# Optimization experiments

Hardware: AMD Instinct MI355X
Metric: run time of the kernel (lower is better)

## Reference

```python
import jax, jax.numpy as jnp
import numpy as np

NW, NS, E = 50000, 10000, 100000
H, C = 6, 300            # heads, out_channels (word_size)
DIN_S, DIN_W = 640, 300  # sentence_size, word_size
DHID = 2048              # FFN hidden


def setup_inputs() -> dict:
    key = jax.random.key(0)
    ks = jax.random.split(key, 12)
    Hw = jax.random.normal(ks[0], (NW, DIN_W), dtype=jnp.float32)
    Hs = jax.random.normal(ks[1], (NS, DIN_S), dtype=jnp.float32)
    src = jax.random.randint(ks[2], (E,), 0, NS)
    dst = jax.random.randint(ks[3], (E,), 0, NW)
    s2w = jnp.stack([src, dst]).astype(jnp.int64)  # [2, E] edge_index
    # GATConv params (bipartite): lin_src, lin_dst, att_src, att_dst, bias
    Wsrc = jax.random.normal(ks[4], (H * C, DIN_S), dtype=jnp.float32) / np.sqrt(DIN_S)
    Wdst = jax.random.normal(ks[5], (H * C, DIN_W), dtype=jnp.float32) / np.sqrt(DIN_W)
    att_src = jax.random.normal(ks[6], (H, C), dtype=jnp.float32) / np.sqrt(C)
    att_dst = jax.random.normal(ks[7], (H, C), dtype=jnp.float32) / np.sqrt(C)
    bias_gat = jnp.zeros((H * C,), dtype=jnp.float32)
    # FFN params: Linear(1800 -> 2048), Linear(2048 -> 300)
    W1 = jax.random.normal(ks[8], (DHID, H * C), dtype=jnp.float32) / np.sqrt(H * C)
    b1 = jnp.zeros((DHID,), dtype=jnp.float32)
    W2 = jax.random.normal(ks[9], (DIN_W, DHID), dtype=jnp.float32) / np.sqrt(DHID)
    b2 = jnp.zeros((DIN_W,), dtype=jnp.float32)
    return dict(Hw=Hw, Hs=Hs, s2w=s2w, Wsrc=Wsrc, Wdst=Wdst, att_src=att_src,
                att_dst=att_dst, bias_gat=bias_gat, W1=W1, b1=b1, W2=W2, b2=b2)


def reference(Hw, Hs, s2w, Wsrc, Wdst, att_src, att_dst, bias_gat, W1, b1, W2, b2):
    nw = Hw.shape[0]
    src, dst = s2w[0], s2w[1]
    h, c = att_src.shape
    # edge-wise linear transforms (done node-wise, then gathered)
    xs = (Hs @ Wsrc.T).reshape(-1, h, c)   # [Ns, H, C]
    xd = (Hw @ Wdst.T).reshape(-1, h, c)   # [Nw, H, C]
    a_s = jnp.einsum('nhc,hc->nh', xs, att_src)  # [Ns, H]
    a_d = jnp.einsum('nhc,hc->nh', xd, att_dst)  # [Nw, H]
    alpha = a_s[src] + a_d[dst]                  # [E, H]
    alpha = jnp.where(alpha > 0, alpha, 0.2 * alpha)  # leaky_relu(0.2)
    # segment softmax over edges grouped by destination word
    m = jax.ops.segment_max(alpha, dst, num_segments=nw)      # [Nw, H]
    ex = jnp.exp(alpha - m[dst])                               # [E, H]
    den = jax.ops.segment_sum(ex, dst, num_segments=nw)       # [Nw, H]
    w = ex / den[dst]                                          # [E, H]
    msg = xs[src] * w[:, :, None]                              # [E, H, C]
    agg = jax.ops.segment_sum(msg, dst, num_segments=nw)      # [Nw, H, C]
    Uw = agg.reshape(nw, h * c) + bias_gat                     # concat heads + bias
    # activation (elu), dropout treated as identity (deterministic reference)
    Uw = jax.nn.elu(Uw)
    # FFN with residual to Hw
    out = (Uw @ W1.T + b1) @ W2.T + b2 + Hw
    return out
```

## Files before the change

### kernel.cpp

```cpp
#include <hip/hip_runtime.h>
#include <hip/hip_bf16.h>
#include <math.h>

#define NWn 50000
#define NSn 10000
#define NEn 100000
#define Hn  6
#define DWn 300
#define DSn 640
#define DHn 2048
#define HCn 1800
#define HCp 1824
#define CHUNK 10000
#define ENC_NEGINF 0x007FFFFFu

typedef short bf16x8 __attribute__((ext_vector_type(8)));
typedef float f32x4  __attribute__((ext_vector_type(4)));

__device__ __forceinline__ unsigned enc_ord(float f) {
  unsigned u = __float_as_uint(f);
  return (u & 0x80000000u) ? ~u : (u | 0x80000000u);
}
__device__ __forceinline__ float dec_ord(unsigned u) {
  unsigned v = (u & 0x80000000u) ? (u ^ 0x80000000u) : ~u;
  return __uint_as_float(v);
}
__device__ __forceinline__ float eluf(float x) { return x > 0.0f ? x : expm1f(x); }
__device__ __forceinline__ float b2f(short s) {
  return __uint_as_float(((unsigned)(unsigned short)s) << 16);
}
__device__ __forceinline__ short f2b(float f) {
  __hip_bfloat16 h = __float2bfloat16(f);
  return *(short*)&h;
}

__device__ __forceinline__ int ld_src(const int* s32, int e, int f) {
  return f ? s32[2 * e] : s32[e];
}
__device__ __forceinline__ int ld_dst(const int* s32, int e, int f) {
  return f ? s32[2 * NEn + 2 * e] : s32[NEn + e];
}

__global__ __launch_bounds__(256) void k_init(unsigned* m_enc, float* den, int* deg,
                                              int* cur, int* flag, float* Vs, float* Vd) {
  int i = blockIdx.x * 256 + threadIdx.x;
  if (i < NWn * Hn) { m_enc[i] = ENC_NEGINF; den[i] = 0.0f; }
  if (i < NWn) { deg[i] = 0; cur[i] = 0; }
  if (i < Hn * DSn) Vs[i] = 0.f;
  if (i < Hn * DWn) Vd[i] = 0.f;
  if (i == 0) *flag = 1;
}

__global__ __launch_bounds__(256) void k_detect(const int* __restrict__ s32, int* flag) {
  int j = threadIdx.x;
  if (s32[2 * j + 1] != 0) atomicAnd(flag, 0);
}

__global__ __launch_bounds__(256) void k_initout(const float* __restrict__ bc,
    const float* __restrict__ Hw, float* __restrict__ outp) {
  int i4 = blockIdx.x * 256 + threadIdx.x;
  if (i4 >= NWn * DWn / 4) return;
  int c4 = (i4 % 75) * 4;
  float4 b = *(const float4*)&bc[c4];
  float4 h = *(const float4*)&Hw[(size_t)i4 * 4];
  float4 o = make_float4(b.x + h.x, b.y + h.y, b.z + h.z, b.w + h.w);
  *(float4*)&outp[(size_t)i4 * 4] = o;
}

__global__ __launch_bounds__(256) void k_cvt(const float* __restrict__ src,
    __hip_bfloat16* __restrict__ dst, int n4) {
  int i = blockIdx.x * 256 + threadIdx.x;
  if (i >= n4) return;
  float4 v = *(const float4*)&src[(size_t)i * 4];
  __hip_bfloat16 o[4] = {__float2bfloat16(v.x), __float2bfloat16(v.y),
                         __float2bfloat16(v.z), __float2bfloat16(v.w)};
  *(ulong1*)&dst[(size_t)i * 4] = *(ulong1*)o;
}

__global__ __launch_bounds__(256) void k_tcvt(const float* __restrict__ W1,
    __hip_bfloat16* __restrict__ W1t) {
  __shared__ __hip_bfloat16 T[64][65];
  int tid = threadIdx.x;
  int tx = tid & 15, ty = tid >> 4;
  int c0 = blockIdx.x * 64;
  int r0 = blockIdx.y * 64;
  #pragma unroll
  for (int rr = 0; rr < 4; ++rr) {
    int sr = r0 + rr * 16 + ty;
    int sc = c0 + tx * 4;
    float4 v;
    if (sc + 3 < HCn) {
      v = *(const float4*)&W1[(size_t)sr * HCn + sc];
    } else {
      v.x = (sc + 0 < HCn) ? W1[(size_t)sr * HCn + sc + 0] : 0.f;
      v.y = (sc + 1 < HCn) ? W1[(size_t)sr * HCn + sc + 1] : 0.f;
      v.z = (sc + 2 < HCn) ? W1[(size_t)sr * HCn + sc + 2] : 0.f;
      v.w = (sc + 3 < HCn) ? W1[(size_t)sr * HCn + sc + 3] : 0.f;
    }
    T[tx * 4 + 0][rr * 16 + ty] = __float2bfloat16(v.x);
    T[tx * 4 + 1][rr * 16 + ty] = __float2bfloat16(v.y);
    T[tx * 4 + 2][rr * 16 + ty] = __float2bfloat16(v.z);
    T[tx * 4 + 3][rr * 16 + ty] = __float2bfloat16(v.w);
  }
  __syncthreads();
  #pragma unroll
  for (int ww = 0; ww < 4; ++ww) {
    int dl = ww * 16 + ty;
    int dr = c0 + dl;
    if (dr >= HCn) continue;
    __hip_bfloat16 o[4] = {T[dl][tx * 4 + 0], T[dl][tx * 4 + 1],
                           T[dl][tx * 4 + 2], T[dl][tx * 4 + 3]};
    *(uint2*)&W1t[(size_t)dr * DHn + r0 + tx * 4] = *(uint2*)o;
  }
}

#define VCC 6
__global__ __launch_bounds__(256) void k_vsd(const float* __restrict__ Wsrc,
    const float* __restrict__ Wdst, const float* __restrict__ att_src,
    const float* __restrict__ att_dst, float* __restrict__ Vs, float* __restrict__ Vd) {
  int b = blockIdx.x;
  bool isD = b >= Hn * VCC;
  int bb = isD ? b - Hn * VCC : b;
  int h = bb / VCC, cc = bb % VCC;
  int cbeg = h * 300 + cc * 50, cend = cbeg + 50;
  if (!isD) {
    for (int k = threadIdx.x; k < DSn; k += 256) {
      float s = 0.f;
      for (int c = cbeg; c < cend; ++c)
        s = fmaf(att_src[c], Wsrc[(size_t)c * DSn + k], s);
      unsafeAtomicAdd(&Vs[h * DSn + k], s);
    }
  } else {
    for (int k = threadIdx.x; k < DWn; k += 256) {
      float s = 0.f;
      for (int c = cbeg; c < cend; ++c)
        s = fmaf(att_dst[c], Wdst[(size_t)c * DWn + k], s);
      unsafeAtomicAdd(&Vd[h * DWn + k], s);
    }
  }
}

__global__ __launch_bounds__(256) void k_rowdot(const float* __restrict__ X,
    const float* __restrict__ V, float* __restrict__ outv, int nrows, int K) {
  extern __shared__ float VL[];
  for (int i = threadIdx.x; i < Hn * K; i += 256) VL[i] = V[i];
  __syncthreads();
  int row = blockIdx.x * 4 + (threadIdx.x >> 6);
  int lane = threadIdx.x & 63;
  if (row >= nrows) return;
  float acc[Hn] = {0.f, 0.f, 0.f, 0.f, 0.f, 0.f};
  const float* xr = X + (size_t)row * K;
  for (int k = lane; k < K; k += 64) {
    float x = xr[k];
    #pragma unroll
    for (int h = 0; h < Hn; ++h) acc[h] = fmaf(x, VL[h * K + k], acc[h]);
  }
  #pragma unroll
  for (int h = 0; h < Hn; ++h) {
    float v = acc[h];
    for (int ofs = 32; ofs > 0; ofs >>= 1) v += __shfl_down(v, ofs);
    if (lane == 0) outv[(size_t)row * Hn + h] = v;
  }
}

__global__ __launch_bounds__(256) void k_bc(const float* __restrict__ W2,
    const float* __restrict__ b1, const float* __restrict__ b2, float* __restrict__ bc) {
  int j = blockIdx.x * 4 + (threadIdx.x >> 6);
  int lane = threadIdx.x & 63;
  if (j >= DWn) return;
  float s = 0.f;
  for (int t = lane; t < DHn; t += 64) s = fmaf(W2[(size_t)j * DHn + t], b1[t], s);
  for (int ofs = 32; ofs > 0; ofs >>= 1) s += __shfl_down(s, ofs);
  if (lane == 0) bc[j] = s + b2[j];
}

template <int EPI>
__global__ __launch_bounds__(256) void k_mfma(
    const __hip_bfloat16* __restrict__ A, const __hip_bfloat16* __restrict__ B,
    void* __restrict__ Cout, int M, int N, int K, int lda, int ldb, int ldc,
    const float* __restrict__ bc, const float* __restrict__ Hw, int rowbase) {
  __shared__ short As[2][128 * 32];
  __shared__ short Bs[2][128 * 32];
  int tid = threadIdx.x, lane = tid & 63, wid = tid >> 6;
  int wr = wid >> 1, wc = wid & 1;
  int nwg = (int)(gridDim.x * gridDim.y);
  int wg = (int)(blockIdx.y * gridDim.x + blockIdx.x);
  int q = nwg >> 3, r = nwg & 7;
  int xcd = wg & 7, idx = wg >> 3;
  int swz = (xcd < r) ? (xcd * (q + 1) + idx) : (r * (q + 1) + (xcd - r) * q + idx);
  int m0 = (swz / (int)gridDim.x) * 128, n0 = (swz % (int)gridDim.x) * 128;
  int z = blockIdx.z;
  int ksp = K / (int)gridDim.z;
  int kbeg = z * ksp;
  int nt = ksp / 32;

  auto STAGE = [&](int buf, int kk) {
    #pragma unroll
    for (int i = 0; i < 2; ++i) {
      int slotbase = wid * 128 + i * 64;
      int s = slotbase + lane;
      int row = s >> 2, kq = (s & 3) ^ ((row >> 1) & 3);
      int gm = m0 + row; if (gm > M - 1) gm = M - 1;
      const __hip_bfloat16* gsa = A + (size_t)gm * lda + kk + kq * 8;
      __builtin_amdgcn_global_load_lds(
          (const __attribute__((address_space(1))) void*)gsa,
          (__attribute__((address_space(3))) void*)&As[buf][slotbase * 8], 16, 0, 0);
      int gn = n0 + row; if (gn > N - 1) gn = N - 1;
      const __hip_bfloat16* gsb = B + (size_t)gn * ldb + kk + kq * 8;
      __builtin_amdgcn_global_load_lds(
          (const __attribute__((address_space(1))) void*)gsb,
          (__attribute__((address_space(3))) void*)&Bs[buf][slotbase * 8], 16, 0, 0);
    }
  };

  f32x4 acc[4][4] = {};
  STAGE(0, kbeg);
  int cur = 0;
  for (int t = 0; t < nt; ++t) {
    __builtin_amdgcn_s_barrier();
    if (t + 1 < nt) {
      STAGE(cur ^ 1, kbeg + (t + 1) * 32);
      asm volatile("s_waitcnt vmcnt(4)" ::: "memory");
    } else {
      asm volatile("s_waitcnt vmcnt(0)" ::: "memory");
    }
    __builtin_amdgcn_s_barrier();
    __builtin_amdgcn_sched_barrier(0);
    bf16x8 af[4], bfr[4];
    int kqw = lane >> 4;
    #pragma unroll
    for (int mf = 0; mf < 4; ++mf) {
      int ra = wr * 64 + mf * 16 + (lane & 15);
      af[mf] = *(bf16x8*)&As[cur][(ra * 4 + (kqw ^ ((ra >> 1) & 3))) * 8];
    }
    #pragma unroll
    for (int nf = 0; nf < 4; ++nf) {
      int rb = wc * 64 + nf * 16 + (lane & 15);
      bfr[nf] = *(bf16x8*)&Bs[cur][(rb * 4 + (kqw ^ ((rb >> 1) & 3))) * 8];
    }
    #pragma unroll
    for (int mf = 0; mf < 4; ++mf)
      #pragma unroll
      for (int nf = 0; nf < 4; ++nf)
        acc[mf][nf] = __builtin_amdgcn_mfma_f32_16x16x32_bf16(af[mf], bfr[nf],
                                                              acc[mf][nf], 0, 0, 0);
    cur ^= 1;
  }
  #pragma unroll
  for (int mf = 0; mf < 4; ++mf) {
    int gmb = m0 + wr * 64 + mf * 16 + (lane >> 4) * 4;
    #pragma unroll
    for (int nf = 0; nf < 4; ++nf) {
      int gn = n0 + wc * 64 + nf * 16 + (lane & 15);
      if (gn >= N) continue;
      #pragma unroll
      for (int r4 = 0; r4 < 4; ++r4) {
        int gm = gmb + r4;
        if (gm >= M) continue;
        if (EPI == 0) {
          ((__hip_bfloat16*)Cout)[(size_t)gm * ldc + gn] = __float2bfloat16(acc[mf][nf][r4]);
        } else if (EPI == 1) {
          size_t grow = (size_t)(rowbase + gm);
          ((float*)Cout)[grow * ldc + gn] = acc[mf][nf][r4] + bc[gn] + Hw[grow * ldc + gn];
        } else if (EPI == 2) {
          ((float*)Cout)[((size_t)z * M + gm) * ldc + gn] = acc[mf][nf][r4];
        } else {
          size_t grow = (size_t)(rowbase + gm);
          unsafeAtomicAdd(&((float*)Cout)[grow * ldc + gn], acc[mf][nf][r4]);
        }
      }
    }
  }
}

__global__ __launch_bounds__(256) void k_wc_reduce(const float* __restrict__ part,
    __hip_bfloat16* __restrict__ Wcb) {
  int i = blockIdx.x * 256 + threadIdx.x;
  if (i >= DWn * HCp) return;
  int m = i / HCp, n = i % HCp;
  float s = 0.f;
  if (n < HCn) {
    #pragma unroll
    for (int s8 = 0; s8 < 8; ++s8)
      s += part[((size_t)s8 * DWn + m) * HCp + n];
  }
  Wcb[i] = __float2bfloat16(s);
}

__global__ __launch_bounds__(256) void k_alpha(const int* __restrict__ s32,
    const int* __restrict__ flag, const float* __restrict__ a_s,
    const float* __restrict__ a_d, float* __restrict__ alpha,
    unsigned* __restrict__ m_enc, int* __restrict__ deg) {
  int e = blockIdx.x * 256 + threadIdx.x;
  if (e >= NEn) return;
  int f = *flag;
  int s = ld_src(s32, e, f), d = ld_dst(s32, e, f);
  atomicAdd(&deg[d], 1);
  #pragma unroll
  for (int h = 0; h < Hn; ++h) {
    float av = a_s[s * Hn + h] + a_d[d * Hn + h];
    float lr = av > 0.f ? av : 0.2f * av;
    alpha[(size_t)e * Hn + h] = lr;
    atomicMax(&m_enc[d * Hn + h], enc_ord(lr));
  }
}

__global__ __launch_bounds__(256) void k_ex(const int* __restrict__ s32,
    const int* __restrict__ flag, float* __restrict__ wgt,
    const unsigned* __restrict__ m_enc, float* __restrict__ den) {
  int e = blockIdx.x * 256 + threadIdx.x;
  if (e >= NEn) return;
  int d = ld_dst(s32, e, *flag);
  #pragma unroll
  for (int h = 0; h < Hn; ++h) {
    float mx = dec_ord(m_enc[d * Hn + h]);
    float exv = expf(wgt[(size_t)e * Hn + h] - mx);
    wgt[(size_t)e * Hn + h] = exv;
    unsafeAtomicAdd(&den[d * Hn + h], exv);
  }
}

__global__ __launch_bounds__(256) void k_scan1(const int* __restrict__ deg,
    int* __restrict__ off, int* __restrict__ bsum) {
  __shared__ int sh[256];
  int i = blockIdx.x * 256 + threadIdx.x;
  int v = (i < NWn) ? deg[i] : 0;
  sh[threadIdx.x] = v;
  __syncthreads();
  for (int ofs = 1; ofs < 256; ofs <<= 1) {
    int t = (threadIdx.x >= ofs) ? sh[threadIdx.x - ofs] : 0;
    __syncthreads();
    sh[threadIdx.x] += t;
    __syncthreads();
  }
  if (i < NWn) off[i] = sh[threadIdx.x] - v;
  if (threadIdx.x == 255) bsum[blockIdx.x] = sh[255];
}

__global__ __launch_bounds__(256) void k_scan2(const int* __restrict__ bsum,
    int* __restrict__ boff, int nb) {
  __shared__ int sh[256];
  int v = (threadIdx.x < nb) ? bsum[threadIdx.x] : 0;
  sh[threadIdx.x] = v;
  __syncthreads();
  for (int ofs = 1; ofs < 256; ofs <<= 1) {
    int t = (threadIdx.x >= ofs) ? sh[threadIdx.x - ofs] : 0;
    __syncthreads();
    sh[threadIdx.x] += t;
    __syncthreads();
  }
  if (threadIdx.x < nb) boff[threadIdx.x] = sh[threadIdx.x] - v;
}

__global__ __launch_bounds__(256) void k_scan3(int* __restrict__ off,
    const int* __restrict__ boff) {
  int i = blockIdx.x * 256 + threadIdx.x;
  if (i < NWn) off[i] += boff[blockIdx.x];
}

__global__ __launch_bounds__(256) void k_fill(const int* __restrict__ s32,
    const int* __restrict__ flag, const int* __restrict__ off,
    int* __restrict__ cur, int* __restrict__ eid) {
  int e = blockIdx.x * 256 + threadIdx.x;
  if (e >= NEn) return;
  int d = ld_dst(s32, e, *flag);
  int pos = off[d] + atomicAdd(&cur[d], 1);
  eid[pos] = e;
}

__global__ __launch_bounds__(256) void k_agg(const int* __restrict__ s32,
    const int* __restrict__ flag, const int* __restrict__ eid,
    const int* __restrict__ off, const __hip_bfloat16* __restrict__ xs,
    const float* __restrict__ wgt, const float* __restrict__ den,
    const float* __restrict__ bias_gat, __hip_bfloat16* __restrict__ aggc,
    int rowbase) {
  int d = rowbase + blockIdx.x;
  int c0 = threadIdx.x * 8;
  if (c0 >= HCp) return;
  if (c0 >= HCn) {
    bf16x8 zz = {};
    *(bf16x8*)&aggc[(size_t)blockIdx.x * HCp + c0] = zz;
    return;
  }
  int f = *flag;
  int start = off[d];
  int end = (d == NWn - 1) ? NEn : off[d + 1];
  int hlo = c0 / 300, hhi = (c0 + 7) / 300;
  int split = (hlo == hhi) ? 8 : (hhi * 300 - c0);
  float acc[8] = {};
  for (int p = start; p < end; ++p) {
    int e = eid[p];
    int s = ld_src(s32, e, f);
    bf16x8 x = *(const bf16x8*)&xs[(size_t)s * HCn + c0];
    float wlo = wgt[(size_t)e * Hn + hlo];
    float whi = wgt[(size_t)e * Hn + hhi];
    #pragma unroll
    for (int j = 0; j < 8; ++j)
      acc[j] = fmaf((j < split) ? wlo : whi, b2f(x[j]), acc[j]);
  }
  float dlo = den[(size_t)d * Hn + hlo];
  float dhi = den[(size_t)d * Hn + hhi];
  float ilo = dlo > 0.f ? 1.0f / dlo : 0.f;
  float ihi = dhi > 0.f ? 1.0f / dhi : 0.f;
  float4 b0 = *(const float4*)&bias_gat[c0];
  float4 b1v = *(const float4*)&bias_gat[c0 + 4];
  float bb[8] = {b0.x, b0.y, b0.z, b0.w, b1v.x, b1v.y, b1v.z, b1v.w};
  bf16x8 o;
  #pragma unroll
  for (int j = 0; j < 8; ++j)
    o[j] = f2b(eluf(acc[j] * ((j < split) ? ilo : ihi) + bb[j]));
  *(bf16x8*)&aggc[(size_t)blockIdx.x * HCp + c0] = o;
}

extern "C" void kernel_launch(void* const* d_in, const int* in_sizes, int n_in,
                              void* d_out, int out_size, void* d_ws, size_t ws_size,
                              hipStream_t stream) {
  const float* Hw       = (const float*)d_in[0];
  const float* Hs       = (const float*)d_in[1];
  const int*   s2w      = (const int*)d_in[2];
  const float* Wsrc     = (const float*)d_in[3];
  const float* Wdst     = (const float*)d_in[4];
  const float* att_src  = (const float*)d_in[5];
  const float* att_dst  = (const float*)d_in[6];
  const float* bias_gat = (const float*)d_in[7];
  const float* W1       = (const float*)d_in[8];
  const float* b1       = (const float*)d_in[9];
  const float* W2       = (const float*)d_in[10];
  const float* b2       = (const float*)d_in[11];
  float* out = (float*)d_out;

  char* ws = (char*)d_ws;
  size_t o = 0;
  auto alloc = [&](size_t bytes) {
    size_t cur = o;
    o = (o + bytes + 255) & ~(size_t)255;
    return cur;
  };
  __hip_bfloat16* xs    = (__hip_bfloat16*)(ws + alloc(2ull * NSn * HCn));
  __hip_bfloat16* Wsrcb = (__hip_bfloat16*)(ws + alloc(2ull * HCn * DSn));
  __hip_bfloat16* Wcb   = (__hip_bfloat16*)(ws + alloc(2ull * DWn * HCp));
  float*    bc    = (float*)(ws + alloc(sizeof(float) * DWn));
  float*    Vs    = (float*)(ws + alloc(sizeof(float) * Hn * DSn));
  float*    Vd    = (float*)(ws + alloc(sizeof(float) * Hn * DWn));
  float*    a_s   = (float*)(ws + alloc(sizeof(float) * (size_t)NSn * Hn));
  float*    a_d   = (float*)(ws + alloc(sizeof(float) * (size_t)NWn * Hn));
  float*    wgt   = (float*)(ws + alloc(sizeof(float) * (size_t)NEn * Hn));
  unsigned* m_enc = (unsigned*)(ws + alloc(sizeof(unsigned) * (size_t)NWn * Hn));
  float*    den   = (float*)(ws + alloc(sizeof(float) * (size_t)NWn * Hn));
  int*      deg   = (int*)(ws + alloc(sizeof(int) * NWn));
  int*      offr  = (int*)(ws + alloc(sizeof(int) * NWn));
  int*      cur   = (int*)(ws + alloc(sizeof(int) * NWn));
  int*      eid   = (int*)(ws + alloc(sizeof(int) * NEn));
  int*      bsum  = (int*)(ws + alloc(sizeof(int) * 256));
  int*      boff  = (int*)(ws + alloc(sizeof(int) * 256));
  int*      flag  = (int*)(ws + alloc(sizeof(int) * 64));
  size_t region = o;
  size_t ro = region;
  auto ralloc = [&](size_t bytes) {
    size_t cur2 = ro;
    ro = (ro + bytes + 255) & ~(size_t)255;
    return cur2;
  };
  __hip_bfloat16* Hsb = (__hip_bfloat16*)(ws + ralloc(2ull * NSn * DSn));
  __hip_bfloat16* W2b = (__hip_bfloat16*)(ws + ralloc(2ull * DWn * DHn));
  __hip_bfloat16* W1t = (__hip_bfloat16*)(ws + ralloc(2ull * HCn * DHn));
  float*          WcP = (float*)(ws + ralloc(4ull * 8 * DWn * HCp));
  size_t region_small_end = ro;
  size_t big_end = region + 2ull * NWn * HCp;
  bool bigpath = (big_end <= ws_size);
  __hip_bfloat16* aggc;
  if (bigpath) {
    aggc = (__hip_bfloat16*)(ws + region);
  } else {
    o = region_small_end;
    aggc = (__hip_bfloat16*)(ws + alloc(2ull * CHUNK * HCp));
    if (o > ws_size) return;
  }
  (void)in_sizes; (void)n_in; (void)out_size;

  const int NWB = (NWn + 255) / 256;

  k_init<<<dim3((NWn * Hn + 255) / 256), dim3(256), 0, stream>>>(
      m_enc, den, deg, cur, flag, Vs, Vd);
  k_detect<<<dim3(1), dim3(256), 0, stream>>>(s2w, flag);
  k_cvt<<<dim3((NSn * DSn / 4 + 255) / 256), dim3(256), 0, stream>>>(Hs, Hsb, NSn * DSn / 4);
  k_cvt<<<dim3((HCn * DSn / 4 + 255) / 256), dim3(256), 0, stream>>>(Wsrc, Wsrcb, HCn * DSn / 4);
  k_cvt<<<dim3((DWn * DHn / 4 + 255) / 256), dim3(256), 0, stream>>>(W2, W2b, DWn * DHn / 4);
  k_tcvt<<<dim3((HCn + 63) / 64, DHn / 64), dim3(256), 0, stream>>>(W1, W1t);
  k_vsd<<<dim3(2 * Hn * VCC), dim3(256), 0, stream>>>(
      Wsrc, Wdst, att_src, att_dst, Vs, Vd);
  k_bc<<<dim3((DWn + 3) / 4), dim3(256), 0, stream>>>(W2, b1, b2, bc);
  if (!bigpath)
    k_initout<<<dim3((NWn * DWn / 4 + 255) / 256), dim3(256), 0, stream>>>(bc, Hw, out);
  k_mfma<2><<<dim3((HCn + 127) / 128, (DWn + 127) / 128, 8), dim3(256), 0, stream>>>(
      W2b, W1t, WcP, DWn, HCn, DHn, DHn, DHn, HCp, nullptr, nullptr, 0);
  k_wc_reduce<<<dim3((DWn * HCp + 255) / 256), dim3(256), 0, stream>>>(WcP, Wcb);
  k_rowdot<<<dim3((NSn + 3) / 4), dim3(256), Hn * DSn * sizeof(float), stream>>>(
      Hs, Vs, a_s, NSn, DSn);
  k_rowdot<<<dim3((NWn + 3) / 4), dim3(256), Hn * DWn * sizeof(float), stream>>>(
      Hw, Vd, a_d, NWn, DWn);
  k_mfma<0><<<dim3((HCn + 127) / 128, (NSn + 127) / 128, 1), dim3(256), 0, stream>>>(
      Hsb, Wsrcb, xs, NSn, HCn, DSn, DSn, DSn, HCn, nullptr, nullptr, 0);
  k_alpha<<<dim3((NEn + 255) / 256), dim3(256), 0, stream>>>(
      s2w, flag, a_s, a_d, wgt, m_enc, deg);
  k_ex<<<dim3((NEn + 255) / 256), dim3(256), 0, stream>>>(s2w, flag, wgt, m_enc, den);
  k_scan1<<<dim3(NWB), dim3(256), 0, stream>>>(deg, offr, bsum);
  k_scan2<<<dim3(1), dim3(256), 0, stream>>>(bsum, boff, NWB);
  k_scan3<<<dim3(NWB), dim3(256), 0, stream>>>(offr, boff);
  k_fill<<<dim3((NEn + 255) / 256), dim3(256), 0, stream>>>(s2w, flag, offr, cur, eid);
  if (bigpath) {
    k_agg<<<dim3(NWn), dim3(256), 0, stream>>>(
        s2w, flag, eid, offr, xs, wgt, den, bias_gat, aggc, 0);
    k_mfma<1><<<dim3((DWn + 127) / 128, (NWn + 127) / 128, 1), dim3(256), 0, stream>>>(
        aggc, Wcb, out, NWn, DWn, HCp, HCp, HCp, DWn, bc, Hw, 0);
  } else {
    for (int c = 0; c < NWn / CHUNK; ++c) {
      int rowbase = c * CHUNK;
      k_agg<<<dim3(CHUNK), dim3(256), 0, stream>>>(
          s2w, flag, eid, offr, xs, wgt, den, bias_gat, aggc, rowbase);
      k_mfma<3><<<dim3((DWn + 127) / 128, (CHUNK + 127) / 128, 3), dim3(256), 0, stream>>>(
          aggc, Wcb, out, CHUNK, DWn, HCp, HCp, HCp, DWn, nullptr, nullptr, rowbase);
    }
  }
}
```

Baseline: 568.5 us.

## Pre-pack aggregation and weight matrices into MFMA fragment layout for final GEMM

The aggregation kernel and the weight reduction now write their bf16 outputs straight into a fragment-packed layout that matches the MFMA 16x16x32 operand order. A new GEMM kernel loads operands directly from global memory with no LDS staging and no barriers. It applies the bias+residual epilogue itself, which replaces the split-K atomic-add path and the separate output-init kernel. The trade-off is that there is no LDS reuse, so each wave re-reads its A/B fragments from global memory and relies on the caches. The first GEMM also loses its XCD swizzle.

```diff
diff --git a/kernel.cpp b/kernel.cpp
--- a/kernel.cpp
+++ b/kernel.cpp
@@ -11,6 +11,8 @@
 #define DHn 2048
 #define HCn 1800
 #define HCp 1824
+#define K32 57
+#define NFB 19
 #define CHUNK 10000
 #define ENC_NEGINF 0x007FFFFFu
 
@@ -54,17 +56,6 @@
 __global__ __launch_bounds__(256) void k_detect(const int* __restrict__ s32, int* flag) {
   int j = threadIdx.x;
   if (s32[2 * j + 1] != 0) atomicAnd(flag, 0);
-}
-
-__global__ __launch_bounds__(256) void k_initout(const float* __restrict__ bc,
-    const float* __restrict__ Hw, float* __restrict__ outp) {
-  int i4 = blockIdx.x * 256 + threadIdx.x;
-  if (i4 >= NWn * DWn / 4) return;
-  int c4 = (i4 % 75) * 4;
-  float4 b = *(const float4*)&bc[c4];
-  float4 h = *(const float4*)&Hw[(size_t)i4 * 4];
-  float4 o = make_float4(b.x + h.x, b.y + h.y, b.z + h.z, b.w + h.w);
-  *(float4*)&outp[(size_t)i4 * 4] = o;
 }
 
 __global__ __launch_bounds__(256) void k_cvt(const float* __restrict__ src,
@@ -177,23 +168,16 @@
 template <int EPI>
 __global__ __launch_bounds__(256) void k_mfma(
     const __hip_bfloat16* __restrict__ A, const __hip_bfloat16* __restrict__ B,
-    void* __restrict__ Cout, int M, int N, int K, int lda, int ldb, int ldc,
-    const float* __restrict__ bc, const float* __restrict__ Hw, int rowbase) {
+    void* __restrict__ Cout, int M, int N, int K, int lda, int ldb, int ldc) {
   __shared__ short As[2][128 * 32];
   __shared__ short Bs[2][128 * 32];
   int tid = threadIdx.x, lane = tid & 63, wid = tid >> 6;
   int wr = wid >> 1, wc = wid & 1;
-  int nwg = (int)(gridDim.x * gridDim.y);
-  int wg = (int)(blockIdx.y * gridDim.x + blockIdx.x);
-  int q = nwg >> 3, r = nwg & 7;
-  int xcd = wg & 7, idx = wg >> 3;
-  int swz = (xcd < r) ? (xcd * (q + 1) + idx) : (r * (q + 1) + (xcd - r) * q + idx);
-  int m0 = (swz / (int)gridDim.x) * 128, n0 = (swz % (int)gridDim.x) * 128;
+  int m0 = blockIdx.y * 128, n0 = blockIdx.x * 128;
   int z = blockIdx.z;
   int ksp = K / (int)gridDim.z;
   int kbeg = z * ksp;
   int nt = ksp / 32;
-
   auto STAGE = [&](int buf, int kk) {
     #pragma unroll
     for (int i = 0; i < 2; ++i) {
@@ -212,7 +196,6 @@
           (__attribute__((address_space(3))) void*)&Bs[buf][slotbase * 8], 16, 0, 0);
     }
   };
-
   f32x4 acc[4][4] = {};
   STAGE(0, kbeg);
   int cur = 0;
@@ -257,34 +240,88 @@
       for (int r4 = 0; r4 < 4; ++r4) {
         int gm = gmb + r4;
         if (gm >= M) continue;
-        if (EPI == 0) {
+        if (EPI == 0)
           ((__hip_bfloat16*)Cout)[(size_t)gm * ldc + gn] = __float2bfloat16(acc[mf][nf][r4]);
-        } else if (EPI == 1) {
-          size_t grow = (size_t)(rowbase + gm);
-          ((float*)Cout)[grow * ldc + gn] = acc[mf][nf][r4] + bc[gn] + Hw[grow * ldc + gn];
-        } else if (EPI == 2) {
+        else
           ((float*)Cout)[((size_t)z * M + gm) * ldc + gn] = acc[mf][nf][r4];
-        } else {
-          size_t grow = (size_t)(rowbase + gm);
-          unsafeAtomicAdd(&((float*)Cout)[grow * ldc + gn], acc[mf][nf][r4]);
-        }
       }
     }
   }
 }
 
+__global__ __launch_bounds__(256) void k_mfma_pa(
+    const __hip_bfloat16* __restrict__ Apk, const __hip_bfloat16* __restrict__ Bpk,
+    float* __restrict__ Cout, int M, int maxAf,
+    const float* __restrict__ bc, const float* __restrict__ Hw, int rowbase) {
+  int tid = threadIdx.x, lane = tid & 63, wid = tid >> 6;
+  int wr = wid >> 1, wc = wid & 1;
+  int nwg = (int)(gridDim.x * gridDim.y);
+  int wg = (int)(blockIdx.y * gridDim.x + blockIdx.x);
+  int q = nwg >> 3, r = nwg & 7;
+  int xcd = wg & 7, idx = wg >> 3;
+  int swz = (xcd < r) ? (xcd * (q + 1) + idx) : (r * (q + 1) + (xcd - r) * q + idx);
+  int m0 = (swz / (int)gridDim.x) * 128, n0 = (swz % (int)gridDim.x) * 128;
+  const short* Ab = (const short*)Apk;
+  const short* Bb = (const short*)Bpk;
+  int ra16[4], cb16[4];
+  #pragma unroll
+  for (int mf = 0; mf < 4; ++mf) {
+    int v = (m0 >> 4) + wr * 4 + mf;
+    ra16[mf] = v > maxAf ? maxAf : v;
+  }
+  #pragma unroll
+  for (int nf = 0; nf < 4; ++nf) {
+    int v = (n0 >> 4) + wc * 4 + nf;
+    cb16[nf] = v > (NFB - 1) ? (NFB - 1) : v;
+  }
+  f32x4 acc[4][4] = {};
+  for (int ks = 0; ks < K32; ++ks) {
+    bf16x8 af[4], bfv[4];
+    #pragma unroll
+    for (int mf = 0; mf < 4; ++mf)
+      af[mf] = *(const bf16x8*)&Ab[((size_t)ra16[mf] * K32 + ks) * 512 + lane * 8];
+    #pragma unroll
+    for (int nf = 0; nf < 4; ++nf)
+      bfv[nf] = *(const bf16x8*)&Bb[((size_t)cb16[nf] * K32 + ks) * 512 + lane * 8];
+    #pragma unroll
+    for (int mf = 0; mf < 4; ++mf)
+      #pragma unroll
+      for (int nf = 0; nf < 4; ++nf)
+        acc[mf][nf] = __builtin_amdgcn_mfma_f32_16x16x32_bf16(af[mf], bfv[nf],
+                                                              acc[mf][nf], 0, 0, 0);
+  }
+  #pragma unroll
+  for (int mf = 0; mf < 4; ++mf) {
+    int gmb = m0 + wr * 64 + mf * 16 + (lane >> 4) * 4;
+    #pragma unroll
+    for (int nf = 0; nf < 4; ++nf) {
+      int gn = n0 + wc * 64 + nf * 16 + (lane & 15);
+      if (gn >= DWn) continue;
+      #pragma unroll
+      for (int r4 = 0; r4 < 4; ++r4) {
+        int gm = gmb + r4;
+        if (gm >= M) continue;
+        size_t grow = (size_t)(rowbase + gm);
+        Cout[grow * DWn + gn] = acc[mf][nf][r4] + bc[gn] + Hw[grow * DWn + gn];
+      }
+    }
+  }
+}
+
 __global__ __launch_bounds__(256) void k_wc_reduce(const float* __restrict__ part,
-    __hip_bfloat16* __restrict__ Wcb) {
+    __hip_bfloat16* __restrict__ Bpk) {
   int i = blockIdx.x * 256 + threadIdx.x;
-  if (i >= DWn * HCp) return;
+  if (i >= 16 * NFB * HCp) return;
   int m = i / HCp, n = i % HCp;
   float s = 0.f;
-  if (n < HCn) {
+  if (m < DWn && n < HCn) {
     #pragma unroll
     for (int s8 = 0; s8 < 8; ++s8)
       s += part[((size_t)s8 * DWn + m) * HCp + n];
   }
-  Wcb[i] = __float2bfloat16(s);
+  size_t frag = (size_t)(m >> 4) * K32 + (n >> 5);
+  int lane = ((n >> 3) & 3) * 16 + (m & 15);
+  Bpk[frag * 512 + lane * 8 + (n & 7)] = __float2bfloat16(s);
 }
 
 __global__ __launch_bounds__(256) void k_alpha(const int* __restrict__ s32,
@@ -372,14 +409,18 @@
     const int* __restrict__ flag, const int* __restrict__ eid,
     const int* __restrict__ off, const __hip_bfloat16* __restrict__ xs,
     const float* __restrict__ wgt, const float* __restrict__ den,
-    const float* __restrict__ bias_gat, __hip_bfloat16* __restrict__ aggc,
+    const float* __restrict__ bias_gat, __hip_bfloat16* __restrict__ aggP,
     int rowbase) {
-  int d = rowbase + blockIdx.x;
+  int rloc = blockIdx.x;
+  int d = rowbase + rloc;
   int c0 = threadIdx.x * 8;
   if (c0 >= HCp) return;
+  size_t frag = (size_t)(rloc >> 4) * K32 + (c0 >> 5);
+  int plane = ((c0 >> 3) & 3) * 16 + (rloc & 15);
+  short* dst = (short*)aggP + frag * 512 + plane * 8;
   if (c0 >= HCn) {
     bf16x8 zz = {};
-    *(bf16x8*)&aggc[(size_t)blockIdx.x * HCp + c0] = zz;
+    *(bf16x8*)dst = zz;
     return;
   }
   int f = *flag;
@@ -409,7 +450,7 @@
   #pragma unroll
   for (int j = 0; j < 8; ++j)
     o[j] = f2b(eluf(acc[j] * ((j < split) ? ilo : ihi) + bb[j]));
-  *(bf16x8*)&aggc[(size_t)blockIdx.x * HCp + c0] = o;
+  *(bf16x8*)dst = o;
 }
 
 extern "C" void kernel_launch(void* const* d_in, const int* in_sizes, int n_in,
@@ -438,7 +479,7 @@
   };
   __hip_bfloat16* xs    = (__hip_bfloat16*)(ws + alloc(2ull * NSn * HCn));
   __hip_bfloat16* Wsrcb = (__hip_bfloat16*)(ws + alloc(2ull * HCn * DSn));
-  __hip_bfloat16* Wcb   = (__hip_bfloat16*)(ws + alloc(2ull * DWn * HCp));
+  __hip_bfloat16* Bpk   = (__hip_bfloat16*)(ws + alloc(2ull * NFB * K32 * 512));
   float*    bc    = (float*)(ws + alloc(sizeof(float) * DWn));
   float*    Vs    = (float*)(ws + alloc(sizeof(float) * Hn * DSn));
   float*    Vd    = (float*)(ws + alloc(sizeof(float) * Hn * DWn));
@@ -490,17 +531,15 @@
   k_vsd<<<dim3(2 * Hn * VCC), dim3(256), 0, stream>>>(
       Wsrc, Wdst, att_src, att_dst, Vs, Vd);
   k_bc<<<dim3((DWn + 3) / 4), dim3(256), 0, stream>>>(W2, b1, b2, bc);
-  if (!bigpath)
-    k_initout<<<dim3((NWn * DWn / 4 + 255) / 256), dim3(256), 0, stream>>>(bc, Hw, out);
   k_mfma<2><<<dim3((HCn + 127) / 128, (DWn + 127) / 128, 8), dim3(256), 0, stream>>>(
-      W2b, W1t, WcP, DWn, HCn, DHn, DHn, DHn, HCp, nullptr, nullptr, 0);
-  k_wc_reduce<<<dim3((DWn * HCp + 255) / 256), dim3(256), 0, stream>>>(WcP, Wcb);
+      W2b, W1t, WcP, DWn, HCn, DHn, DHn, DHn, HCp);
+  k_wc_reduce<<<dim3((16 * NFB * HCp + 255) / 256), dim3(256), 0, stream>>>(WcP, Bpk);
   k_rowdot<<<dim3((NSn + 3) / 4), dim3(256), Hn * DSn * sizeof(float), stream>>>(
       Hs, Vs, a_s, NSn, DSn);
   k_rowdot<<<dim3((NWn + 3) / 4), dim3(256), Hn * DWn * sizeof(float), stream>>>(
       Hw, Vd, a_d, NWn, DWn);
   k_mfma<0><<<dim3((HCn + 127) / 128, (NSn + 127) / 128, 1), dim3(256), 0, stream>>>(
-      Hsb, Wsrcb, xs, NSn, HCn, DSn, DSn, DSn, HCn, nullptr, nullptr, 0);
+      Hsb, Wsrcb, xs, NSn, HCn, DSn, DSn, DSn, HCn);
   k_alpha<<<dim3((NEn + 255) / 256), dim3(256), 0, stream>>>(
       s2w, flag, a_s, a_d, wgt, m_enc, deg);
   k_ex<<<dim3((NEn + 255) / 256), dim3(256), 0, stream>>>(s2w, flag, wgt, m_enc, den);
@@ -511,15 +550,15 @@
   if (bigpath) {
     k_agg<<<dim3(NWn), dim3(256), 0, stream>>>(
         s2w, flag, eid, offr, xs, wgt, den, bias_gat, aggc, 0);
-    k_mfma<1><<<dim3((DWn + 127) / 128, (NWn + 127) / 128, 1), dim3(256), 0, stream>>>(
-        aggc, Wcb, out, NWn, DWn, HCp, HCp, HCp, DWn, bc, Hw, 0);
+    k_mfma_pa<<<dim3(3, (NWn + 127) / 128), dim3(256), 0, stream>>>(
+        aggc, Bpk, out, NWn, NWn / 16 - 1, bc, Hw, 0);
   } else {
     for (int c = 0; c < NWn / CHUNK; ++c) {
       int rowbase = c * CHUNK;
       k_agg<<<dim3(CHUNK), dim3(256), 0, stream>>>(
           s2w, flag, eid, offr, xs, wgt, den, bias_gat, aggc, rowbase);
-      k_mfma<3><<<dim3((DWn + 127) / 128, (CHUNK + 127) / 128, 3), dim3(256), 0, stream>>>(
-          aggc, Wcb, out, CHUNK, DWn, HCp, HCp, HCp, DWn, nullptr, nullptr, rowbase);
-    }
-  }
-}
+      k_mfma_pa<<<dim3(3, (CHUNK + 127) / 128), dim3(256), 0, stream>>>(
+          aggc, Bpk, out, CHUNK, CHUNK / 16 - 1, bc, Hw, rowbase);
+    }
+  }
+}
```

After: 654.5 us. +15.1%, slower.
